# Optimization experiments

Hardware: AMD Instinct MI355X
Metric: run time of the kernel (lower is better)

The kernel has to match this reference:

```python
import jax, jax.numpy as jnp
import numpy as np

K = 5  # kernel_size per pseudo dim (degree-1 open B-spline)


def spline_conv(x, src, dst, edge_attr, W, root, bias, num_nodes):
    """PyG SplineConv: degree-1 open B-spline, dim=2, kernel_size=5, aggr='mean',
    root weight + bias. W: [K*K, in, out], root: [in, out], bias: [out]."""
    v = edge_attr * (K - 1)                      # [E,2] in [0, K-1]
    k = jnp.clip(jnp.floor(v), 0, K - 2)         # [E,2] lower knot per dim
    frac = v - k                                  # [E,2]
    ki = k.astype(jnp.int32)
    # per-dim linear basis and knot indices for the 2 support points
    b = jnp.stack([1.0 - frac, frac], axis=-1)    # [E,2,2] (dim, s)
    idx = ki[..., None] + jnp.arange(2, dtype=jnp.int32)  # [E,2,2]
    # tensor-product over the 2 pseudo dims -> 4 basis/weight-index pairs per edge
    basis = (b[:, 0, :, None] * b[:, 1, None, :]).reshape(-1, 4)        # [E,4]
    wi = (idx[:, 0, :, None] + K * idx[:, 1, None, :]).reshape(-1, 4)   # [E,4]
    # precompute x @ W_k for all 25 kernels, then gather per edge
    XW = jnp.einsum('ni,kio->nko', x, W)          # [N,25,out]
    msg = jnp.einsum('es,eso->eo', basis, XW[src[:, None], wi])  # [E,out]
    agg = jax.ops.segment_sum(msg, dst, num_segments=num_nodes)  # [N,out]
    deg = jax.ops.segment_sum(jnp.ones_like(dst, dtype=x.dtype), dst,
                              num_segments=num_nodes)
    agg = agg / jnp.maximum(deg, 1.0)[:, None]    # mean aggregation
    return agg + x @ root + bias


def setup_inputs() -> dict:
    key = jax.random.key(0)
    ks = jax.random.split(key, 16)
    N, E = 100000, 1600000
    x = jax.random.normal(ks[0], (N, 2), dtype=jnp.float32)
    edge_index = jax.random.randint(ks[1], (2, E), 0, N, dtype=jnp.int32)
    edge_attr = jax.random.uniform(ks[2], (E, 2), dtype=jnp.float32)
    def glorot(k, shape):
        fan = shape[-2] + shape[-1]
        return jax.random.uniform(k, shape, jnp.float32,
                                  -np.sqrt(6.0 / fan), np.sqrt(6.0 / fan))
    W1 = glorot(ks[3], (25, 2, 16));  root1 = glorot(ks[4], (2, 16))
    W2 = glorot(ks[5], (25, 16, 16)); root2 = glorot(ks[6], (16, 16))
    W3 = glorot(ks[7], (25, 16, 16)); root3 = glorot(ks[8], (16, 16))
    b1 = jnp.zeros((16,), jnp.float32)
    b2 = jnp.zeros((16,), jnp.float32)
    b3 = jnp.zeros((16,), jnp.float32)
    fc_w = glorot(ks[9], (16, 1))
    fc_b = jnp.zeros((1,), jnp.float32)
    return {"x": x, "edge_index": edge_index, "edge_attr": edge_attr,
            "W1": W1, "root1": root1, "b1": b1,
            "W2": W2, "root2": root2, "b2": b2,
            "W3": W3, "root3": root3, "b3": b3,
            "fc_w": fc_w, "fc_b": fc_b}


def reference(x, edge_index, edge_attr, W1, root1, b1, W2, root2, b2,
              W3, root3, b3, fc_w, fc_b):
    N = x.shape[0]
    src, dst = edge_index[0], edge_index[1]
    h = jax.nn.relu(spline_conv(x, src, dst, edge_attr, W1, root1, b1, N))
    h = jax.nn.relu(spline_conv(h, src, dst, edge_attr, W2, root2, b2, N))
    h = jax.nn.relu(spline_conv(h, src, dst, edge_attr, W3, root3, b3, N))
    logits = (h @ fc_w + fc_b).squeeze(-1)        # [N]
    return jax.nn.sigmoid(logits)
```

## Files before the change

### kernel.cpp

```cpp
#include <hip/hip_runtime.h>
#include <math.h>


#define KS 5
#define BW 512
#define TILE 4096

typedef _Float16 h2f __attribute__((ext_vector_type(2)));

__device__ __forceinline__ h2f u2h(unsigned u) { return __builtin_bit_cast(h2f, u); }

#if __has_builtin(__builtin_amdgcn_fdot2)
__device__ __forceinline__ float fdot2(h2f a, h2f b, float c) {
    return __builtin_amdgcn_fdot2(a, b, c, false);
}
#else
__device__ __forceinline__ float fdot2(h2f a, h2f b, float c) {
    return c + (float)a[0] * (float)b[0] + (float)a[1] * (float)b[1];
}
#endif

__device__ __forceinline__ unsigned packh2(float lo, float hi) {
    return (unsigned)__builtin_bit_cast(ushort, (_Float16)lo) |
           ((unsigned)__builtin_bit_cast(ushort, (_Float16)hi) << 16);
}

__global__ void bucket_hist_kernel(const int* __restrict__ dst, int* __restrict__ bcnt,
                                   int E, int B) {
    __shared__ int lh[256];
    lh[threadIdx.x] = 0;
    __syncthreads();
    int stride = gridDim.x * blockDim.x;
    for (int e = blockIdx.x * blockDim.x + threadIdx.x; e < E; e += stride)
        atomicAdd(&lh[dst[e] >> 9], 1);
    __syncthreads();
    int c = lh[threadIdx.x];
    if ((int)threadIdx.x < B && c) atomicAdd(&bcnt[threadIdx.x], c);
}

__global__ void bucket_scan_kernel(const int* __restrict__ bcnt, int* __restrict__ bbase,
                                   int* __restrict__ bcursor, int B, int E) {
    __shared__ int sh[256];
    int v = ((int)threadIdx.x < B) ? bcnt[threadIdx.x] : 0;
    sh[threadIdx.x] = v;
    __syncthreads();
    for (int off = 1; off < 256; off <<= 1) {
        int t = (threadIdx.x >= (unsigned)off) ? sh[threadIdx.x - off] : 0;
        __syncthreads();
        sh[threadIdx.x] += t;
        __syncthreads();
    }
    if ((int)threadIdx.x < B) {
        bbase[threadIdx.x] = sh[threadIdx.x] - v;
        bcursor[threadIdx.x] = 0;
    }
    if (threadIdx.x == 0) bbase[B] = E;
}

__global__ __launch_bounds__(256) void bin_kernel(
        const float* __restrict__ eattr, const int* __restrict__ src,
        const int* __restrict__ dst, const int* __restrict__ bbase,
        int* __restrict__ bcursor, uint2* __restrict__ bin, int E) {
    __shared__ int lh[256];
    __shared__ int labs[256];
    __shared__ int lcur[256];
    lh[threadIdx.x] = 0;
    lcur[threadIdx.x] = 0;
    __syncthreads();
    int t0 = blockIdx.x * TILE;
    #pragma unroll
    for (int it = 0; it < TILE / 256; ++it) {
        int e = t0 + it * 256 + threadIdx.x;
        if (e < E) atomicAdd(&lh[dst[e] >> 9], 1);
    }
    __syncthreads();
    {
        int c = lh[threadIdx.x];
        if (c) labs[threadIdx.x] = bbase[threadIdx.x] + atomicAdd(&bcursor[threadIdx.x], c);
    }
    __syncthreads();
    #pragma unroll
    for (int it = 0; it < TILE / 256; ++it) {
        int e = t0 + it * 256 + threadIdx.x;
        if (e < E) {
            float2 ea = reinterpret_cast<const float2*>(eattr)[e];
            float a0 = ea.x * (float)(KS - 1);
            float a1 = ea.y * (float)(KS - 1);
            float k0 = fminf(fmaxf(floorf(a0), 0.0f), (float)(KS - 2));
            float k1 = fminf(fmaxf(floorf(a1), 0.0f), (float)(KS - 2));
            float f0 = a0 - k0, f1 = a1 - k1;
            unsigned w00 = (unsigned)((int)k0 + KS * (int)k1);
            int d = dst[e];
            int b = d >> 9;
            unsigned dloc = (unsigned)(d & 511);
            unsigned w0 = (unsigned)src[e] | ((dloc & 255u) << 17) | (w00 << 25) |
                          ((dloc >> 8) << 30);
            int p = atomicAdd(&lcur[b], 1);
            bin[labs[b] + p] = make_uint2(w0, packh2(f0, f1));
        }
    }
}

__global__ __launch_bounds__(256) void bucket_scatter_kernel(
        const uint2* __restrict__ bin, const int* __restrict__ bbase,
        uint2* __restrict__ epack, int* __restrict__ offs, int N, int E) {
    __shared__ int lcnt[512];
    __shared__ int loff[512];
    __shared__ int lcur[512];
    __shared__ int ssc[256];
    int tid = threadIdx.x;
    int b = blockIdx.x;
    int base = bbase[b];
    int cntb = bbase[b + 1] - base;
    int nbase = b << 9;
    lcnt[tid] = 0; lcnt[tid + 256] = 0;
    lcur[tid] = 0; lcur[tid + 256] = 0;
    __syncthreads();
    for (int r = tid; r < cntb; r += 256) {
        unsigned w0 = bin[base + r].x;
        int dloc = (int)(((w0 >> 17) & 255u) | (((w0 >> 30) & 1u) << 8));
        atomicAdd(&lcnt[dloc], 1);
    }
    __syncthreads();
    int a0 = lcnt[2 * tid], a1 = lcnt[2 * tid + 1];
    ssc[tid] = a0 + a1;
    __syncthreads();
    for (int off = 1; off < 256; off <<= 1) {
        int t = (tid >= off) ? ssc[tid - off] : 0;
        __syncthreads();
        ssc[tid] += t;
        __syncthreads();
    }
    int ex = (tid > 0) ? ssc[tid - 1] : 0;
    loff[2 * tid] = ex;
    loff[2 * tid + 1] = ex + a0;
    __syncthreads();
    for (int i = tid; i < 512; i += 256) {
        int n = nbase + i;
        if (n < N) offs[n] = base + loff[i];
    }
    if (b == 0 && tid == 0) offs[N] = E;
    for (int r = tid; r < cntb; r += 256) {
        uint2 rec = bin[base + r];
        int dloc = (int)(((rec.x >> 17) & 255u) | (((rec.x >> 30) & 1u) << 8));
        int p = atomicAdd(&lcur[dloc], 1);
        epack[base + loff[dloc] + p] = make_uint2(rec.x & 0x3E01FFFFu, rec.y);
    }
}

__global__ __launch_bounds__(256, 8) void csr2_kernel(
        const float* __restrict__ x,
        const uint2* __restrict__ epack,
        const int* __restrict__ offs,
        const float* __restrict__ W,
        const float* __restrict__ root,
        const float* __restrict__ bias,
        ushort* __restrict__ hout,
        int N) {
    __shared__ float Wl[25 * 32];
    for (int idx = threadIdx.x; idx < 25 * 32; idx += blockDim.x) {
        int k = idx >> 5;
        int r = idx & 31;
        int i = r >> 4;
        int o = r & 15;
        Wl[k * 32 + o * 2 + i] = W[idx];
    }
    __syncthreads();

    int t = blockIdx.x * blockDim.x + threadIdx.x;
    if (t >= N * 16) return;
    int o = t & 15;
    int n = t >> 4;
    int row = offs[n], end = offs[n + 1];

    float acc = 0.0f;
    if (row < end) {
        uint2 pk = epack[row];
        float2 xpf = reinterpret_cast<const float2*>(x)[pk.x & 0x1FFFFFFu];
        for (int j = row; j < end; ++j) {
            uint2 cur = pk;
            float2 xv = xpf;
            int jn = (j + 1 < end) ? j + 1 : j;
            pk = epack[jn];
            xpf = reinterpret_cast<const float2*>(x)[pk.x & 0x1FFFFFFu];
            int w00 = (int)((cur.x >> 25) & 31u);
            h2f f = u2h(cur.y);
            float f0 = (float)f[0], f1 = (float)f[1];
            float g0 = 1.0f - f0, g1 = 1.0f - f1;
            float bb[4] = {g0 * g1, f0 * g1, g0 * f1, f0 * f1};
            int wiarr[4] = {w00, w00 + 1, w00 + KS, w00 + KS + 1};
            #pragma unroll
            for (int sp = 0; sp < 4; ++sp) {
                float2 w = *reinterpret_cast<const float2*>(&Wl[wiarr[sp] * 32 + o * 2]);
                acc += bb[sp] * (xv.x * w.x + xv.y * w.y);
            }
        }
    }
    float inv = 1.0f / fmaxf((float)(end - row), 1.0f);
    float2 xn = reinterpret_cast<const float2*>(x)[n];
    acc = acc * inv + xn.x * root[o] + xn.y * root[16 + o] + bias[o];
    hout[t] = __builtin_bit_cast(ushort, (_Float16)fmaxf(acc, 0.0f));
}

__global__ __launch_bounds__(256, 8) void csr16_kernel(
        const ushort* __restrict__ hh,
        const uint2* __restrict__ epack,
        const int* __restrict__ offs,
        const float* __restrict__ W,
        const float* __restrict__ root,
        const float* __restrict__ bias,
        ushort* __restrict__ hout,
        int N) {
    __shared__ unsigned Wl[25 * 192 + 192];
    for (int idx = threadIdx.x; idx < 25 * 128 + 128; idx += blockDim.x) {
        if (idx < 25 * 128) {
            int k = idx >> 7;
            int d = idx & 127;
            int o = d >> 3;
            int j = d & 7;
            int i0 = ((j >> 2) << 3) + ((j & 3) << 1);
            Wl[k * 192 + o * 12 + j] =
                packh2(W[k * 256 + i0 * 16 + o], W[k * 256 + (i0 + 1) * 16 + o]);
        } else {
            int d = idx - 25 * 128;
            int o = d >> 3;
            int j = d & 7;
            int i0 = ((j >> 2) << 3) + ((j & 3) << 1);
            Wl[4800 + o * 12 + j] = packh2(root[i0 * 16 + o], root[(i0 + 1) * 16 + o]);
        }
    }
    __syncthreads();

    int t = blockIdx.x * blockDim.x + threadIdx.x;
    if (t >= N * 16) return;
    int o = t & 15;
    int n = t >> 4;
    int row = offs[n], end = offs[n + 1];
    int s0 = o * 12;

    float acc = 0.0f;
    if (row < end) {
        uint2 pk = epack[row];
        const uint4* hpn = reinterpret_cast<const uint4*>(hh + (size_t)(pk.x & 0x1FFFFFFu) * 16);
        uint4 ha_n = hpn[0], hb_n = hpn[1];
        for (int j = row; j < end; ++j) {
            uint2 cur = pk;
            uint4 ha = ha_n, hb = hb_n;
            int jn = (j + 1 < end) ? j + 1 : j;
            pk = epack[jn];
            const uint4* hp2 = reinterpret_cast<const uint4*>(hh + (size_t)(pk.x & 0x1FFFFFFu) * 16);
            ha_n = hp2[0]; hb_n = hp2[1];
            int w00 = (int)((cur.x >> 25) & 31u);
            h2f f = u2h(cur.y);
            float f0 = (float)f[0], f1 = (float)f[1];
            float g0 = 1.0f - f0, g1 = 1.0f - f1;
            float bb[4] = {g0 * g1, f0 * g1, g0 * f1, f0 * f1};
            int wiarr[4] = {w00, w00 + 1, w00 + KS, w00 + KS + 1};
            #pragma unroll
            for (int sp = 0; sp < 4; ++sp) {
                int kb = wiarr[sp] * 192 + s0;
                uint4 wa = *reinterpret_cast<const uint4*>(&Wl[kb]);
                uint4 wb = *reinterpret_cast<const uint4*>(&Wl[kb + 4]);
                float pA = 0.0f, pB = 0.0f;
                pA = fdot2(u2h(ha.x), u2h(wa.x), pA);
                pA = fdot2(u2h(ha.y), u2h(wa.y), pA);
                pA = fdot2(u2h(ha.z), u2h(wa.z), pA);
                pA = fdot2(u2h(ha.w), u2h(wa.w), pA);
                pB = fdot2(u2h(hb.x), u2h(wb.x), pB);
                pB = fdot2(u2h(hb.y), u2h(wb.y), pB);
                pB = fdot2(u2h(hb.z), u2h(wb.z), pB);
                pB = fdot2(u2h(hb.w), u2h(wb.w), pB);
                acc = fmaf(bb[sp], pA + pB, acc);
            }
        }
    }
    float inv = 1.0f / fmaxf((float)(end - row), 1.0f);
    acc *= inv;
    {
        const uint4* hp = reinterpret_cast<const uint4*>(hh + (size_t)n * 16);
        uint4 ha = hp[0], hb = hp[1];
        uint4 ra = *reinterpret_cast<const uint4*>(&Wl[4800 + s0]);
        uint4 rb = *reinterpret_cast<const uint4*>(&Wl[4800 + s0 + 4]);
        float pA = 0.0f, pB = 0.0f;
        pA = fdot2(u2h(ha.x), u2h(ra.x), pA);
        pA = fdot2(u2h(ha.y), u2h(ra.y), pA);
        pA = fdot2(u2h(ha.z), u2h(ra.z), pA);
        pA = fdot2(u2h(ha.w), u2h(ra.w), pA);
        pB = fdot2(u2h(hb.x), u2h(rb.x), pB);
        pB = fdot2(u2h(hb.y), u2h(rb.y), pB);
        pB = fdot2(u2h(hb.z), u2h(rb.z), pB);
        pB = fdot2(u2h(hb.w), u2h(rb.w), pB);
        acc += pA + pB + bias[o];
    }
    hout[t] = __builtin_bit_cast(ushort, (_Float16)fmaxf(acc, 0.0f));
}

__global__ void fc_kernel(const ushort* __restrict__ h,
                          const float* __restrict__ fcw,
                          const float* __restrict__ fcb,
                          float* __restrict__ out, int N) {
    int n = blockIdx.x * blockDim.x + threadIdx.x;
    if (n >= N) return;
    const uint4* hp = reinterpret_cast<const uint4*>(h + (size_t)n * 16);
    uint4 ha = hp[0], hb = hp[1];
    unsigned dw[8] = {ha.x, ha.y, ha.z, ha.w, hb.x, hb.y, hb.z, hb.w};
    float acc = fcb[0];
    #pragma unroll
    for (int j = 0; j < 8; ++j) {
        h2f p = u2h(dw[j]);
        acc += (float)p[0] * fcw[2 * j] + (float)p[1] * fcw[2 * j + 1];
    }
    out[n] = 1.0f / (1.0f + expf(-acc));
}

__global__ void deg_count_kernel(const int* __restrict__ dst, float* __restrict__ deg, int E) {
    int stride = gridDim.x * blockDim.x;
    for (int e = blockIdx.x * blockDim.x + threadIdx.x; e < E; e += stride)
        atomicAdd(&deg[dst[e]], 1.0f);
}
__global__ void deg_inv_kernel(float* __restrict__ deg, int N) {
    int i = blockIdx.x * blockDim.x + threadIdx.x;
    if (i < N) deg[i] = 1.0f / fmaxf(deg[i], 1.0f);
}
__device__ __forceinline__ void compute_basis(const float* eattr, const int* srcp, int e,
                                              int& s, float b[4], int wi[4]) {
    float2 ea = reinterpret_cast<const float2*>(eattr)[e];
    float a0 = ea.x * (float)(KS - 1);
    float a1 = ea.y * (float)(KS - 1);
    float k0 = fminf(fmaxf(floorf(a0), 0.0f), (float)(KS - 2));
    float k1 = fminf(fmaxf(floorf(a1), 0.0f), (float)(KS - 2));
    float f0 = a0 - k0, f1 = a1 - k1;
    int i0 = (int)k0, i1 = (int)k1;
    int w00 = i0 + KS * i1;
    wi[0] = w00; wi[1] = w00 + 1; wi[2] = w00 + KS; wi[3] = w00 + KS + 1;
    float g0 = 1.0f - f0, g1 = 1.0f - f1;
    b[0] = g0 * g1; b[1] = f0 * g1; b[2] = g0 * f1; b[3] = f0 * f1;
    s = srcp[e];
}
__global__ __launch_bounds__(256) void edge16h_fb(
        const ushort* __restrict__ hh, const int* __restrict__ dst,
        const float* __restrict__ eattr, const int* __restrict__ srcp,
        const float* __restrict__ W, float* __restrict__ agg, int E) {
    __shared__ unsigned Wl[25 * 192];
    for (int idx = threadIdx.x; idx < 25 * 128; idx += blockDim.x) {
        int k = idx >> 7;
        int d = idx & 127;
        int o = d >> 3;
        int j = d & 7;
        int i0 = ((j >> 2) << 3) + ((j & 3) << 1);
        Wl[k * 192 + o * 12 + j] =
            packh2(W[k * 256 + i0 * 16 + o], W[k * 256 + (i0 + 1) * 16 + o]);
    }
    __syncthreads();
    int gs = gridDim.x * blockDim.x;
    int total = E * 16;
    for (int t = blockIdx.x * blockDim.x + threadIdx.x; t < total; t += gs) {
        int e = t >> 4;
        int o = t & 15;
        int s;
        float b[4];
        int wi[4];
        compute_basis(eattr, srcp, e, s, b, wi);
        const uint4* hp = reinterpret_cast<const uint4*>(hh + (size_t)s * 16);
        uint4 ha = hp[0], hb = hp[1];
        float acc = 0.0f;
        #pragma unroll
        for (int sp = 0; sp < 4; ++sp) {
            int kb = wi[sp] * 192 + o * 12;
            uint4 wa = *reinterpret_cast<const uint4*>(&Wl[kb]);
            uint4 wb = *reinterpret_cast<const uint4*>(&Wl[kb + 4]);
            float p = 0.0f;
            p = fdot2(u2h(ha.x), u2h(wa.x), p);
            p = fdot2(u2h(ha.y), u2h(wa.y), p);
            p = fdot2(u2h(ha.z), u2h(wa.z), p);
            p = fdot2(u2h(ha.w), u2h(wa.w), p);
            p = fdot2(u2h(hb.x), u2h(wb.x), p);
            p = fdot2(u2h(hb.y), u2h(wb.y), p);
            p = fdot2(u2h(hb.z), u2h(wb.z), p);
            p = fdot2(u2h(hb.w), u2h(wb.w), p);
            acc = fmaf(b[sp], p, acc);
        }
        atomicAdd(&agg[(size_t)dst[e] * 16 + o], acc);
    }
}
__global__ __launch_bounds__(256) void edge2_fb(
        const float* __restrict__ x, const int* __restrict__ dst,
        const float* __restrict__ eattr, const int* __restrict__ srcp,
        const float* __restrict__ W, float* __restrict__ agg, int E) {
    __shared__ float Wl[25 * 32];
    for (int idx = threadIdx.x; idx < 25 * 32; idx += blockDim.x) {
        int k = idx >> 5;
        int r = idx & 31;
        int i = r >> 4;
        int o = r & 15;
        Wl[k * 32 + o * 2 + i] = W[idx];
    }
    __syncthreads();
    int gs = gridDim.x * blockDim.x;
    int total = E * 16;
    for (int t = blockIdx.x * blockDim.x + threadIdx.x; t < total; t += gs) {
        int e = t >> 4;
        int o = t & 15;
        int s;
        float b[4];
        int wi[4];
        compute_basis(eattr, srcp, e, s, b, wi);
        float2 xv = reinterpret_cast<const float2*>(x)[s];
        float acc = 0.0f;
        #pragma unroll
        for (int sp = 0; sp < 4; ++sp) {
            float2 w = *reinterpret_cast<const float2*>(&Wl[wi[sp] * 32 + o * 2]);
            acc += b[sp] * (xv.x * w.x + xv.y * w.y);
        }
        atomicAdd(&agg[(size_t)dst[e] * 16 + o], acc);
    }
}
__global__ void finalize2h_fb(const float* __restrict__ x, const float* __restrict__ root,
                              const float* __restrict__ bias, const float* __restrict__ invdeg,
                              const float* __restrict__ agg, ushort* __restrict__ hout, int N) {
    int t = blockIdx.x * blockDim.x + threadIdx.x;
    if (t >= N * 16) return;
    int o = t & 15;
    int n = t >> 4;
    float2 xv = reinterpret_cast<const float2*>(x)[n];
    float acc = agg[t] * invdeg[n] + xv.x * root[o] + xv.y * root[16 + o] + bias[o];
    hout[t] = __builtin_bit_cast(ushort, (_Float16)fmaxf(acc, 0.0f));
}
__global__ void finalize16h_fb(const ushort* __restrict__ hin, const float* __restrict__ root,
                               const float* __restrict__ bias, const float* __restrict__ invdeg,
                               const float* __restrict__ agg, ushort* __restrict__ hout, int N) {
    int t = blockIdx.x * blockDim.x + threadIdx.x;
    if (t >= N * 16) return;
    int o = t & 15;
    int n = t >> 4;
    const uint4* hp = reinterpret_cast<const uint4*>(hin + (size_t)n * 16);
    uint4 ha = hp[0], hb = hp[1];
    float acc = agg[t] * invdeg[n] + bias[o];
    unsigned dw[8] = {ha.x, ha.y, ha.z, ha.w, hb.x, hb.y, hb.z, hb.w};
    #pragma unroll
    for (int j = 0; j < 8; ++j) {
        h2f p = u2h(dw[j]);
        acc += (float)p[0] * root[(2 * j) * 16 + o] + (float)p[1] * root[(2 * j + 1) * 16 + o];
    }
    hout[t] = __builtin_bit_cast(ushort, (_Float16)fmaxf(acc, 0.0f));
}

extern "C" void kernel_launch(void* const* d_in, const int* in_sizes, int n_in,
                              void* d_out, int out_size, void* d_ws, size_t ws_size,
                              hipStream_t stream) {
    const float* x      = (const float*)d_in[0];
    const int*   eidx   = (const int*)d_in[1];
    const float* eattr  = (const float*)d_in[2];
    const float* W1     = (const float*)d_in[3];
    const float* root1  = (const float*)d_in[4];
    const float* b1     = (const float*)d_in[5];
    const float* W2     = (const float*)d_in[6];
    const float* root2  = (const float*)d_in[7];
    const float* b2     = (const float*)d_in[8];
    const float* W3     = (const float*)d_in[9];
    const float* root3  = (const float*)d_in[10];
    const float* b3     = (const float*)d_in[11];
    const float* fcw    = (const float*)d_in[12];
    const float* fcb    = (const float*)d_in[13];
    float* out = (float*)d_out;

    const int N = in_sizes[0] / 2;
    const int E = in_sizes[2] / 2;
    const int* src = eidx;
    const int* dst = eidx + E;
    const int BT = 256;
    const int B = (N + BW - 1) / BW;

    char* w = (char*)d_ws;
    size_t off = 0;
    uint2* epack = (uint2*)(w + off); off += (size_t)E * 8;
    uint2* bin   = (uint2*)(w + off); off += (size_t)E * 8;
    int* bcnt    = (int*)(w + off);   off += 256 * 4;
    int* bbase   = (int*)(w + off);   off += 257 * 4;
    int* bcursor = (int*)(w + off);   off += 256 * 4;
    int* offs    = (int*)(w + off);   off += ((size_t)N + 1) * 4; off = (off + 15) & ~(size_t)15;
    ushort* hH1  = (ushort*)(w + off); off += (size_t)N * 32;
    ushort* hH2  = (ushort*)(w + off); off += (size_t)N * 32;
    size_t need_csr = off;

    if (ws_size >= need_csr && B <= 256 && N <= (1 << 17)) {
        hipMemsetAsync(bcnt, 0, 256 * 4, stream);
        bucket_hist_kernel<<<1024, BT, 0, stream>>>(dst, bcnt, E, B);
        bucket_scan_kernel<<<1, 256, 0, stream>>>(bcnt, bbase, bcursor, B, E);
        bin_kernel<<<(E + TILE - 1) / TILE, BT, 0, stream>>>(eattr, src, dst, bbase,
                                                             bcursor, bin, E);
        bucket_scatter_kernel<<<B, 256, 0, stream>>>(bin, bbase, epack, offs, N, E);

        int node_grid = (N * 16 + BT - 1) / BT;
        csr2_kernel<<<node_grid, BT, 0, stream>>>(x, epack, offs, W1, root1, b1, hH1, N);
        csr16_kernel<<<node_grid, BT, 0, stream>>>(hH1, epack, offs, W2, root2, b2, hH2, N);
        csr16_kernel<<<node_grid, BT, 0, stream>>>(hH2, epack, offs, W3, root3, b3, hH1, N);
        fc_kernel<<<(N + BT - 1) / BT, BT, 0, stream>>>(hH1, fcw, fcb, out, N);
    } else {
        float* agg = (float*)d_ws;
        float* deg = agg + (size_t)N * 16;
        size_t f17 = ((size_t)N * 17 + 7) & ~(size_t)7;
        ushort* fH1 = (ushort*)((float*)d_ws + f17);
        ushort* fH2 = fH1 + (size_t)N * 16;
        const int EG = 2048;
        int node_grid = (N * 16 + BT - 1) / BT;

        hipMemsetAsync(deg, 0, (size_t)N * 4, stream);
        deg_count_kernel<<<2048, BT, 0, stream>>>(dst, deg, E);
        deg_inv_kernel<<<(N + BT - 1) / BT, BT, 0, stream>>>(deg, N);

        hipMemsetAsync(agg, 0, (size_t)N * 64, stream);
        edge2_fb<<<EG, BT, 0, stream>>>(x, dst, eattr, src, W1, agg, E);
        finalize2h_fb<<<node_grid, BT, 0, stream>>>(x, root1, b1, deg, agg, fH1, N);

        hipMemsetAsync(agg, 0, (size_t)N * 64, stream);
        edge16h_fb<<<EG, BT, 0, stream>>>(fH1, dst, eattr, src, W2, agg, E);
        finalize16h_fb<<<node_grid, BT, 0, stream>>>(fH1, root2, b2, deg, agg, fH2, N);

        hipMemsetAsync(agg, 0, (size_t)N * 64, stream);
        edge16h_fb<<<EG, BT, 0, stream>>>(fH2, dst, eattr, src, W3, agg, E);
        finalize16h_fb<<<node_grid, BT, 0, stream>>>(fH2, root3, b3, deg, agg, fH1, N);

        fc_kernel<<<(N + BT - 1) / BT, BT, 0, stream>>>(fH1, fcw, fcb, out, N);
    }
}
```

Measured before the change: 331.2 us.

## Precompute per-node XW table for 16-wide layers and gather it per edge

Adds a pass that computes x·W_k for all 25 spline kernels plus the root weight for every node and stores them in fp16, in a buffer that reuses the bin scratch area. The layer-2/3 aggregation kernels then gather four precomputed scalars per edge instead of doing 32 fp16 dot products per edge. This trades per-edge compute for an extra write of about 83 MB per layer and scattered 2-byte gathers. The csr2 and csr16 kernels also lose their next-edge feature prefetch, and the old paths are kept as fallbacks.

```diff
diff --git a/kernel.cpp b/kernel.cpp
--- a/kernel.cpp
+++ b/kernel.cpp
@@ -174,31 +174,138 @@
     int row = offs[n], end = offs[n + 1];
 
     float acc = 0.0f;
+    uint2 pk = epack[(row < end) ? row : 0];
+    for (int j = row; j < end; ++j) {
+        uint2 cur = pk;
+        int jn = j + 1;
+        pk = epack[(jn < end) ? jn : j];
+        int s = (int)(cur.x & 0x1FFFFFFu);
+        int w00 = (int)((cur.x >> 25) & 31u);
+        h2f f = u2h(cur.y);
+        float f0 = (float)f[0], f1 = (float)f[1];
+        float g0 = 1.0f - f0, g1 = 1.0f - f1;
+        float bb[4] = {g0 * g1, f0 * g1, g0 * f1, f0 * f1};
+        int wiarr[4] = {w00, w00 + 1, w00 + KS, w00 + KS + 1};
+        float2 xv = reinterpret_cast<const float2*>(x)[s];
+        #pragma unroll
+        for (int sp = 0; sp < 4; ++sp) {
+            float2 w = *reinterpret_cast<const float2*>(&Wl[wiarr[sp] * 32 + o * 2]);
+            acc += bb[sp] * (xv.x * w.x + xv.y * w.y);
+        }
+    }
+    float inv = 1.0f / fmaxf((float)(end - row), 1.0f);
+    float2 xn = reinterpret_cast<const float2*>(x)[n];
+    acc = acc * inv + xn.x * root[o] + xn.y * root[16 + o] + bias[o];
+    hout[t] = __builtin_bit_cast(ushort, (_Float16)fmaxf(acc, 0.0f));
+}
+
+__global__ __launch_bounds__(256, 8) void xw16_kernel(
+        const ushort* __restrict__ hh,
+        const float* __restrict__ W,
+        const float* __restrict__ root,
+        ushort* __restrict__ XW,
+        int N) {
+    __shared__ unsigned Wl[25 * 192 + 192];
+    for (int idx = threadIdx.x; idx < 25 * 128 + 128; idx += blockDim.x) {
+        if (idx < 25 * 128) {
+            int k = idx >> 7;
+            int d = idx & 127;
+            int o = d >> 3;
+            int j = d & 7;
+            int i0 = ((j >> 2) << 3) + ((j & 3) << 1);
+            Wl[k * 192 + o * 12 + j] =
+                packh2(W[k * 256 + i0 * 16 + o], W[k * 256 + (i0 + 1) * 16 + o]);
+        } else {
+            int d = idx - 25 * 128;
+            int o = d >> 3;
+            int j = d & 7;
+            int i0 = ((j >> 2) << 3) + ((j & 3) << 1);
+            Wl[4800 + o * 12 + j] = packh2(root[i0 * 16 + o], root[(i0 + 1) * 16 + o]);
+        }
+    }
+    __syncthreads();
+
+    int t = blockIdx.x * blockDim.x + threadIdx.x;
+    if (t >= N * 16) return;
+    int o = t & 15;
+    int n = t >> 4;
+    int s0 = o * 12;
+
+    const uint4* hp = reinterpret_cast<const uint4*>(hh + (size_t)n * 16);
+    uint4 ha = hp[0], hb = hp[1];
+    ushort* xw = XW + (size_t)n * 416 + o;
+
+    #pragma unroll 5
+    for (int k = 0; k < 25; ++k) {
+        int kb = k * 192 + s0;
+        uint4 wa = *reinterpret_cast<const uint4*>(&Wl[kb]);
+        uint4 wb = *reinterpret_cast<const uint4*>(&Wl[kb + 4]);
+        float pA = 0.0f, pB = 0.0f;
+        pA = fdot2(u2h(ha.x), u2h(wa.x), pA);
+        pA = fdot2(u2h(ha.y), u2h(wa.y), pA);
+        pA = fdot2(u2h(ha.z), u2h(wa.z), pA);
+        pA = fdot2(u2h(ha.w), u2h(wa.w), pA);
+        pB = fdot2(u2h(hb.x), u2h(wb.x), pB);
+        pB = fdot2(u2h(hb.y), u2h(wb.y), pB);
+        pB = fdot2(u2h(hb.z), u2h(wb.z), pB);
+        pB = fdot2(u2h(hb.w), u2h(wb.w), pB);
+        xw[k * 16] = __builtin_bit_cast(ushort, (_Float16)(pA + pB));
+    }
+    {
+        uint4 ra = *reinterpret_cast<const uint4*>(&Wl[4800 + s0]);
+        uint4 rb = *reinterpret_cast<const uint4*>(&Wl[4800 + s0 + 4]);
+        float pA = 0.0f, pB = 0.0f;
+        pA = fdot2(u2h(ha.x), u2h(ra.x), pA);
+        pA = fdot2(u2h(ha.y), u2h(ra.y), pA);
+        pA = fdot2(u2h(ha.z), u2h(ra.z), pA);
+        pA = fdot2(u2h(ha.w), u2h(ra.w), pA);
+        pB = fdot2(u2h(hb.x), u2h(rb.x), pB);
+        pB = fdot2(u2h(hb.y), u2h(rb.y), pB);
+        pB = fdot2(u2h(hb.z), u2h(rb.z), pB);
+        pB = fdot2(u2h(hb.w), u2h(rb.w), pB);
+        xw[400] = __builtin_bit_cast(ushort, (_Float16)(pA + pB));
+    }
+}
+
+__global__ __launch_bounds__(256, 8) void csr16x_kernel(
+        const ushort* __restrict__ XW,
+        const uint2* __restrict__ epack,
+        const int* __restrict__ offs,
+        const float* __restrict__ bias,
+        ushort* __restrict__ hout,
+        int N) {
+    int t = blockIdx.x * blockDim.x + threadIdx.x;
+    if (t >= N * 16) return;
+    int o = t & 15;
+    int n = t >> 4;
+    int row = offs[n], end = offs[n + 1];
+
+    float acc = 0.0f;
     if (row < end) {
         uint2 pk = epack[row];
-        float2 xpf = reinterpret_cast<const float2*>(x)[pk.x & 0x1FFFFFFu];
         for (int j = row; j < end; ++j) {
             uint2 cur = pk;
-            float2 xv = xpf;
             int jn = (j + 1 < end) ? j + 1 : j;
             pk = epack[jn];
-            xpf = reinterpret_cast<const float2*>(x)[pk.x & 0x1FFFFFFu];
+            int s = (int)(cur.x & 0x1FFFFFFu);
             int w00 = (int)((cur.x >> 25) & 31u);
             h2f f = u2h(cur.y);
             float f0 = (float)f[0], f1 = (float)f[1];
             float g0 = 1.0f - f0, g1 = 1.0f - f1;
-            float bb[4] = {g0 * g1, f0 * g1, g0 * f1, f0 * f1};
-            int wiarr[4] = {w00, w00 + 1, w00 + KS, w00 + KS + 1};
-            #pragma unroll
-            for (int sp = 0; sp < 4; ++sp) {
-                float2 w = *reinterpret_cast<const float2*>(&Wl[wiarr[sp] * 32 + o * 2]);
-                acc += bb[sp] * (xv.x * w.x + xv.y * w.y);
-            }
+            const ushort* xp = XW + (size_t)s * 416 + w00 * 16 + o;
+            float v0 = (float)__builtin_bit_cast(_Float16, xp[0]);
+            float v1 = (float)__builtin_bit_cast(_Float16, xp[16]);
+            float v2 = (float)__builtin_bit_cast(_Float16, xp[80]);
+            float v3 = (float)__builtin_bit_cast(_Float16, xp[96]);
+            acc = fmaf(g0 * g1, v0, acc);
+            acc = fmaf(f0 * g1, v1, acc);
+            acc = fmaf(g0 * f1, v2, acc);
+            acc = fmaf(f0 * f1, v3, acc);
         }
     }
     float inv = 1.0f / fmaxf((float)(end - row), 1.0f);
-    float2 xn = reinterpret_cast<const float2*>(x)[n];
-    acc = acc * inv + xn.x * root[o] + xn.y * root[16 + o] + bias[o];
+    float rootv = (float)__builtin_bit_cast(_Float16, XW[(size_t)n * 416 + 400 + o]);
+    acc = acc * inv + rootv + bias[o];
     hout[t] = __builtin_bit_cast(ushort, (_Float16)fmaxf(acc, 0.0f));
 }
 
@@ -239,39 +346,35 @@
     int s0 = o * 12;
 
     float acc = 0.0f;
-    if (row < end) {
-        uint2 pk = epack[row];
-        const uint4* hpn = reinterpret_cast<const uint4*>(hh + (size_t)(pk.x & 0x1FFFFFFu) * 16);
-        uint4 ha_n = hpn[0], hb_n = hpn[1];
-        for (int j = row; j < end; ++j) {
-            uint2 cur = pk;
-            uint4 ha = ha_n, hb = hb_n;
-            int jn = (j + 1 < end) ? j + 1 : j;
-            pk = epack[jn];
-            const uint4* hp2 = reinterpret_cast<const uint4*>(hh + (size_t)(pk.x & 0x1FFFFFFu) * 16);
-            ha_n = hp2[0]; hb_n = hp2[1];
-            int w00 = (int)((cur.x >> 25) & 31u);
-            h2f f = u2h(cur.y);
-            float f0 = (float)f[0], f1 = (float)f[1];
-            float g0 = 1.0f - f0, g1 = 1.0f - f1;
-            float bb[4] = {g0 * g1, f0 * g1, g0 * f1, f0 * f1};
-            int wiarr[4] = {w00, w00 + 1, w00 + KS, w00 + KS + 1};
-            #pragma unroll
-            for (int sp = 0; sp < 4; ++sp) {
-                int kb = wiarr[sp] * 192 + s0;
-                uint4 wa = *reinterpret_cast<const uint4*>(&Wl[kb]);
-                uint4 wb = *reinterpret_cast<const uint4*>(&Wl[kb + 4]);
-                float pA = 0.0f, pB = 0.0f;
-                pA = fdot2(u2h(ha.x), u2h(wa.x), pA);
-                pA = fdot2(u2h(ha.y), u2h(wa.y), pA);
-                pA = fdot2(u2h(ha.z), u2h(wa.z), pA);
-                pA = fdot2(u2h(ha.w), u2h(wa.w), pA);
-                pB = fdot2(u2h(hb.x), u2h(wb.x), pB);
-                pB = fdot2(u2h(hb.y), u2h(wb.y), pB);
-                pB = fdot2(u2h(hb.z), u2h(wb.z), pB);
-                pB = fdot2(u2h(hb.w), u2h(wb.w), pB);
-                acc = fmaf(bb[sp], pA + pB, acc);
-            }
+    uint2 pk = epack[(row < end) ? row : 0];
+    for (int j = row; j < end; ++j) {
+        uint2 cur = pk;
+        int jn = j + 1;
+        pk = epack[(jn < end) ? jn : j];
+        int s = (int)(cur.x & 0x1FFFFFFu);
+        int w00 = (int)((cur.x >> 25) & 31u);
+        h2f f = u2h(cur.y);
+        float f0 = (float)f[0], f1 = (float)f[1];
+        float g0 = 1.0f - f0, g1 = 1.0f - f1;
+        float bb[4] = {g0 * g1, f0 * g1, g0 * f1, f0 * f1};
+        int wiarr[4] = {w00, w00 + 1, w00 + KS, w00 + KS + 1};
+        const uint4* hp = reinterpret_cast<const uint4*>(hh + (size_t)s * 16);
+        uint4 ha = hp[0], hb = hp[1];
+        #pragma unroll
+        for (int sp = 0; sp < 4; ++sp) {
+            int kb = wiarr[sp] * 192 + s0;
+            uint4 wa = *reinterpret_cast<const uint4*>(&Wl[kb]);
+            uint4 wb = *reinterpret_cast<const uint4*>(&Wl[kb + 4]);
+            float p = 0.0f;
+            p = fdot2(u2h(ha.x), u2h(wa.x), p);
+            p = fdot2(u2h(ha.y), u2h(wa.y), p);
+            p = fdot2(u2h(ha.z), u2h(wa.z), p);
+            p = fdot2(u2h(ha.w), u2h(wa.w), p);
+            p = fdot2(u2h(hb.x), u2h(wb.x), p);
+            p = fdot2(u2h(hb.y), u2h(wb.y), p);
+            p = fdot2(u2h(hb.z), u2h(wb.z), p);
+            p = fdot2(u2h(hb.w), u2h(wb.w), p);
+            acc = fmaf(bb[sp], p, acc);
         }
     }
     float inv = 1.0f / fmaxf((float)(end - row), 1.0f);
@@ -281,16 +384,16 @@
         uint4 ha = hp[0], hb = hp[1];
         uint4 ra = *reinterpret_cast<const uint4*>(&Wl[4800 + s0]);
         uint4 rb = *reinterpret_cast<const uint4*>(&Wl[4800 + s0 + 4]);
-        float pA = 0.0f, pB = 0.0f;
-        pA = fdot2(u2h(ha.x), u2h(ra.x), pA);
-        pA = fdot2(u2h(ha.y), u2h(ra.y), pA);
-        pA = fdot2(u2h(ha.z), u2h(ra.z), pA);
-        pA = fdot2(u2h(ha.w), u2h(ra.w), pA);
-        pB = fdot2(u2h(hb.x), u2h(rb.x), pB);
-        pB = fdot2(u2h(hb.y), u2h(rb.y), pB);
-        pB = fdot2(u2h(hb.z), u2h(rb.z), pB);
-        pB = fdot2(u2h(hb.w), u2h(rb.w), pB);
-        acc += pA + pB + bias[o];
+        float p = 0.0f;
+        p = fdot2(u2h(ha.x), u2h(ra.x), p);
+        p = fdot2(u2h(ha.y), u2h(ra.y), p);
+        p = fdot2(u2h(ha.z), u2h(ra.z), p);
+        p = fdot2(u2h(ha.w), u2h(ra.w), p);
+        p = fdot2(u2h(hb.x), u2h(rb.x), p);
+        p = fdot2(u2h(hb.y), u2h(rb.y), p);
+        p = fdot2(u2h(hb.z), u2h(rb.z), p);
+        p = fdot2(u2h(hb.w), u2h(rb.w), p);
+        acc += p + bias[o];
     }
     hout[t] = __builtin_bit_cast(ushort, (_Float16)fmaxf(acc, 0.0f));
 }
@@ -474,53 +577,83 @@
     char* w = (char*)d_ws;
     size_t off = 0;
     uint2* epack = (uint2*)(w + off); off += (size_t)E * 8;
-    uint2* bin   = (uint2*)(w + off); off += (size_t)E * 8;
-    int* bcnt    = (int*)(w + off);   off += 256 * 4;
-    int* bbase   = (int*)(w + off);   off += 257 * 4;
-    int* bcursor = (int*)(w + off);   off += 256 * 4;
-    int* offs    = (int*)(w + off);   off += ((size_t)N + 1) * 4; off = (off + 15) & ~(size_t)15;
-    ushort* hH1  = (ushort*)(w + off); off += (size_t)N * 32;
-    ushort* hH2  = (ushort*)(w + off); off += (size_t)N * 32;
-    size_t need_csr = off;
-
-    if (ws_size >= need_csr && B <= 256 && N <= (1 << 17)) {
-        hipMemsetAsync(bcnt, 0, 256 * 4, stream);
-        bucket_hist_kernel<<<1024, BT, 0, stream>>>(dst, bcnt, E, B);
-        bucket_scan_kernel<<<1, 256, 0, stream>>>(bcnt, bbase, bcursor, B, E);
-        bin_kernel<<<(E + TILE - 1) / TILE, BT, 0, stream>>>(eattr, src, dst, bbase,
-                                                             bcursor, bin, E);
-        bucket_scatter_kernel<<<B, 256, 0, stream>>>(bin, bbase, epack, offs, N, E);
-
-        int node_grid = (N * 16 + BT - 1) / BT;
-        csr2_kernel<<<node_grid, BT, 0, stream>>>(x, epack, offs, W1, root1, b1, hH1, N);
-        csr16_kernel<<<node_grid, BT, 0, stream>>>(hH1, epack, offs, W2, root2, b2, hH2, N);
-        csr16_kernel<<<node_grid, BT, 0, stream>>>(hH2, epack, offs, W3, root3, b3, hH1, N);
-        fc_kernel<<<(N + BT - 1) / BT, BT, 0, stream>>>(hH1, fcw, fcb, out, N);
-    } else {
-        float* agg = (float*)d_ws;
-        float* deg = agg + (size_t)N * 16;
-        size_t f17 = ((size_t)N * 17 + 7) & ~(size_t)7;
-        ushort* fH1 = (ushort*)((float*)d_ws + f17);
-        ushort* fH2 = fH1 + (size_t)N * 16;
-        const int EG = 2048;
-        int node_grid = (N * 16 + BT - 1) / BT;
-
-        hipMemsetAsync(deg, 0, (size_t)N * 4, stream);
-        deg_count_kernel<<<2048, BT, 0, stream>>>(dst, deg, E);
-        deg_inv_kernel<<<(N + BT - 1) / BT, BT, 0, stream>>>(deg, N);
-
-        hipMemsetAsync(agg, 0, (size_t)N * 64, stream);
-        edge2_fb<<<EG, BT, 0, stream>>>(x, dst, eattr, src, W1, agg, E);
-        finalize2h_fb<<<node_grid, BT, 0, stream>>>(x, root1, b1, deg, agg, fH1, N);
-
-        hipMemsetAsync(agg, 0, (size_t)N * 64, stream);
-        edge16h_fb<<<EG, BT, 0, stream>>>(fH1, dst, eattr, src, W2, agg, E);
-        finalize16h_fb<<<node_grid, BT, 0, stream>>>(fH1, root2, b2, deg, agg, fH2, N);
-
-        hipMemsetAsync(agg, 0, (size_t)N * 64, stream);
-        edge16h_fb<<<EG, BT, 0, stream>>>(fH2, dst, eattr, src, W3, agg, E);
-        finalize16h_fb<<<node_grid, BT, 0, stream>>>(fH2, root3, b3, deg, agg, fH1, N);
-
-        fc_kernel<<<(N + BT - 1) / BT, BT, 0, stream>>>(fH1, fcw, fcb, out, N);
-    }
-}
+    size_t binoff = off;
+    uint2* bin   = (uint2*)(w + binoff);
+    ushort* XW   = (ushort*)(w + binoff);
+    size_t bin_sz = (size_t)E * 8;
+    size_t xw_sz  = (size_t)N * 416 * 2;
+    size_t big = (bin_sz > xw_sz) ? bin_sz : xw_sz;
+    size_t off_small = binoff + bin_sz;
+    size_t off_small_xw = binoff + big;
+
+    auto tail = [&](size_t o0, int** bcnt_, int** bbase_, int** bcursor_,
+                    int** offs_, ushort** hH1_, ushort** hH2_) -> size_t {
+        size_t o = o0;
+        *bcnt_    = (int*)(w + o); o += 256 * 4;
+        *bbase_   = (int*)(w + o); o += 257 * 4;
+        *bcursor_ = (int*)(w + o); o += 256 * 4;
+        *offs_    = (int*)(w + o); o += ((size_t)N + 1) * 4; o = (o + 15) & ~(size_t)15;
+        *hH1_ = (ushort*)(w + o); o += (size_t)N * 32;
+        *hH2_ = (ushort*)(w + o); o += (size_t)N * 32;
+        return o;
+    };
+
+    int *bcnt, *bbase, *bcursor, *offs;
+    ushort *hH1, *hH2;
+    size_t need_xw  = tail(off_small_xw, &bcnt, &bbase, &bcursor, &offs, &hH1, &hH2);
+    bool tier1 = (ws_size >= need_xw && B <= 256 && N <= (1 << 17));
+    if (!tier1) {
+        size_t need_csr = tail(off_small, &bcnt, &bbase, &bcursor, &offs, &hH1, &hH2);
+        if (ws_size >= need_csr && B <= 256 && N <= (1 << 17)) {
+            hipMemsetAsync(bcnt, 0, 256 * 4, stream);
+            bucket_hist_kernel<<<1024, BT, 0, stream>>>(dst, bcnt, E, B);
+            bucket_scan_kernel<<<1, 256, 0, stream>>>(bcnt, bbase, bcursor, B, E);
+            bin_kernel<<<(E + TILE - 1) / TILE, BT, 0, stream>>>(eattr, src, dst, bbase,
+                                                                 bcursor, bin, E);
+            bucket_scatter_kernel<<<B, 256, 0, stream>>>(bin, bbase, epack, offs, N, E);
+            int node_grid = (N * 16 + BT - 1) / BT;
+            csr2_kernel<<<node_grid, BT, 0, stream>>>(x, epack, offs, W1, root1, b1, hH1, N);
+            csr16_kernel<<<node_grid, BT, 0, stream>>>(hH1, epack, offs, W2, root2, b2, hH2, N);
+            csr16_kernel<<<node_grid, BT, 0, stream>>>(hH2, epack, offs, W3, root3, b3, hH1, N);
+            fc_kernel<<<(N + BT - 1) / BT, BT, 0, stream>>>(hH1, fcw, fcb, out, N);
+        } else {
+            float* agg = (float*)d_ws;
+            float* deg = agg + (size_t)N * 16;
+            size_t f17 = ((size_t)N * 17 + 7) & ~(size_t)7;
+            ushort* fH1 = (ushort*)((float*)d_ws + f17);
+            ushort* fH2 = fH1 + (size_t)N * 16;
+            const int EG = 2048;
+            int node_grid = (N * 16 + BT - 1) / BT;
+            hipMemsetAsync(deg, 0, (size_t)N * 4, stream);
+            deg_count_kernel<<<2048, BT, 0, stream>>>(dst, deg, E);
+            deg_inv_kernel<<<(N + BT - 1) / BT, BT, 0, stream>>>(deg, N);
+            hipMemsetAsync(agg, 0, (size_t)N * 64, stream);
+            edge2_fb<<<EG, BT, 0, stream>>>(x, dst, eattr, src, W1, agg, E);
+            finalize2h_fb<<<node_grid, BT, 0, stream>>>(x, root1, b1, deg, agg, fH1, N);
+            hipMemsetAsync(agg, 0, (size_t)N * 64, stream);
+            edge16h_fb<<<EG, BT, 0, stream>>>(fH1, dst, eattr, src, W2, agg, E);
+            finalize16h_fb<<<node_grid, BT, 0, stream>>>(fH1, root2, b2, deg, agg, fH2, N);
+            hipMemsetAsync(agg, 0, (size_t)N * 64, stream);
+            edge16h_fb<<<EG, BT, 0, stream>>>(fH2, dst, eattr, src, W3, agg, E);
+            finalize16h_fb<<<node_grid, BT, 0, stream>>>(fH2, root3, b3, deg, agg, fH1, N);
+            fc_kernel<<<(N + BT - 1) / BT, BT, 0, stream>>>(fH1, fcw, fcb, out, N);
+        }
+        return;
+    }
+
+    hipMemsetAsync(bcnt, 0, 256 * 4, stream);
+    bucket_hist_kernel<<<1024, BT, 0, stream>>>(dst, bcnt, E, B);
+    bucket_scan_kernel<<<1, 256, 0, stream>>>(bcnt, bbase, bcursor, B, E);
+    bin_kernel<<<(E + TILE - 1) / TILE, BT, 0, stream>>>(eattr, src, dst, bbase,
+                                                         bcursor, bin, E);
+    bucket_scatter_kernel<<<B, 256, 0, stream>>>(bin, bbase, epack, offs, N, E);
+
+    int node_grid = (N * 16 + BT - 1) / BT;
+    csr2_kernel<<<node_grid, BT, 0, stream>>>(x, epack, offs, W1, root1, b1, hH1, N);
+    xw16_kernel<<<node_grid, BT, 0, stream>>>(hH1, W2, root2, XW, N);
+    csr16x_kernel<<<node_grid, BT, 0, stream>>>(XW, epack, offs, b2, hH2, N);
+    xw16_kernel<<<node_grid, BT, 0, stream>>>(hH2, W3, root3, XW, N);
+    csr16x_kernel<<<node_grid, BT, 0, stream>>>(XW, epack, offs, b3, hH1, N);
+
+    fc_kernel<<<(N + BT - 1) / BT, BT, 0, stream>>>(hH1, fcw, fcb, out, N);
+}
```

New measurement: 407.4 us. 1.23x slower.
